# Optimization experiments

Measured on AMD Instinct MI355X. Metric: run time of the kernel, lower is better.

The kernel has to match this reference:

```python
import jax, jax.numpy as jnp
import numpy as np

N_NODES = 50000
N_EDGES = 800000
VOCAB = 4096          # node_emb_size
EMB_DIM = 128         # node_emb_dim
HIDDEN = 128          # hidden_dim -> layer1 out = 2*HIDDEN
N_POS = 1024


def gcn_conv(h, edge_index, W, b, n):
    """PyG GCNConv: lin -> add self loops -> sym-normalized scatter-add -> +bias."""
    h = h @ W                                   # [N, out]
    row, col = edge_index[0], edge_index[1]     # source, target
    loop = jnp.arange(n)
    row = jnp.concatenate([row, loop])
    col = jnp.concatenate([col, loop])
    deg = jax.ops.segment_sum(jnp.ones(row.shape[0], dtype=h.dtype), col, num_segments=n)
    dinv = jnp.where(deg > 0, jax.lax.rsqrt(deg), 0.0)
    norm = dinv[row] * dinv[col]                # [E+N]
    msg = h[row] * norm[:, None]                # gather + scale
    return jax.ops.segment_sum(msg, col, num_segments=n) + b


def setup_inputs() -> dict:
    key = jax.random.key(0)
    ks = jax.random.split(key, 10)
    x = jax.random.randint(ks[0], (N_NODES, 1), 0, VOCAB)
    edge_index = jax.random.randint(ks[1], (2, N_EDGES), 0, N_NODES)
    x_position = jax.random.randint(ks[2], (N_POS,), 0, N_NODES)
    # Embedding init: normal(0, emb_dim^-0.5) per initialize_parameters
    emb = jax.random.normal(ks[3], (VOCAB, EMB_DIM), jnp.float32) * EMB_DIM ** -0.5
    # GCN / linear weights (glorot-ish)
    W1 = jax.random.normal(ks[4], (EMB_DIM, 2 * HIDDEN), jnp.float32) * (EMB_DIM ** -0.5)
    b1 = jnp.zeros((2 * HIDDEN,), jnp.float32)
    W2 = jax.random.normal(ks[5], (2 * HIDDEN, HIDDEN), jnp.float32) * ((2 * HIDDEN) ** -0.5)
    b2 = jnp.zeros((HIDDEN,), jnp.float32)
    Wc = jax.random.normal(ks[6], (HIDDEN, VOCAB), jnp.float32) * (HIDDEN ** -0.5)
    bc = jnp.zeros((VOCAB,), jnp.float32)
    return {"x": x, "edge_index": edge_index, "x_position": x_position,
            "emb": emb, "W1": W1, "b1": b1, "W2": W2, "b2": b2, "Wc": Wc, "bc": bc}


def reference(x, edge_index, x_position, emb, W1, b1, W2, b2, Wc, bc):
    n = x.shape[0]
    h = emb[x[:, 0]]                                   # Embedding + squeeze(1)
    h = jax.nn.relu(gcn_conv(h, edge_index, W1, b1, n))
    z = gcn_conv(h, edge_index, W2, b2, n)             # [N, HIDDEN]
    logits = z @ Wc + bc                               # classifier over all nodes
    # embedding stage: mean of classified rows at x_position, keep dim 0
    return jnp.mean(logits[x_position], axis=0, keepdims=True)  # [1, VOCAB]
```

## Files before the change

### kernel.cpp

```cpp
#include <hip/hip_runtime.h>

constexpr int EMB  = 128;
constexpr int H1D  = 256;
constexpr int H2D  = 128;
constexpr int VOC  = 4096;
constexpr int NSL  = 32;

__global__ void k_init(int* cnt, int* count, unsigned int* needed, float* wagg,
                       float* wsum, int* nflag, int* total, int n, int nwords) {
    int i = blockIdx.x * blockDim.x + threadIdx.x;
    if (i < n) { cnt[i] = 0; count[i] = 0; wagg[i] = 0.0f; }
    if (i < nwords) needed[i] = 0u;
    if (i < NSL * H1D) wsum[i] = 0.0f;
    if (i == 0) { *nflag = 0; *total = 0; }
}

__global__ void k_count(const int* __restrict__ xpos, int* count, int np) {
    int p = blockIdx.x * blockDim.x + threadIdx.x;
    if (p < np) atomicAdd(&count[xpos[p]], 1);
}

__global__ void k_hist(const int* __restrict__ row, const int* __restrict__ col,
                       const int* __restrict__ count, int* cnt,
                       unsigned int* needed, int ne) {
    int e = blockIdx.x * blockDim.x + threadIdx.x;
    if (e < ne) {
        int c = col[e];
        atomicAdd(&cnt[c], 1);
        if (count[c] > 0) {
            int r = row[e];
            atomicOr(&needed[r >> 5], 1u << (r & 31));
        }
    }
}

__global__ void k_alloc(const unsigned int* __restrict__ needed,
                        const int* __restrict__ cnt, const int* __restrict__ count,
                        float* wagg, int* needb,
                        int* needlist, int* nflag, int* total,
                        int* offs, int* cursor, int n) {
    int v = blockIdx.x * blockDim.x + threadIdx.x;
    int lane = threadIdx.x & 63;
    int cv = 0;
    bool need = false;
    if (v < n) {
        cv = cnt[v];
        int cc = count[v];
        bool bit = (needed[v >> 5] >> (v & 31)) & 1u;
        bool flag = (cc > 0);
        need = bit || flag;
        needb[v] = need ? 1 : 0;
        if (flag) wagg[v] = (float)cc / ((float)cv + 1.0f);
    }
    int seg = need ? cv : 0;
    int incl = seg;
#pragma unroll
    for (int d = 1; d < 64; d <<= 1) {
        int t = __shfl_up(incl, d);
        if (lane >= d) incl += t;
    }
    int excl = incl - seg;
    int wave_total = __shfl(incl, 63);
    unsigned long long mask = __ballot(need);
    int rank = __popcll(mask & ((1ull << lane) - 1));
    int wcnt = __popcll(mask);
    int base_id = 0, base_off = 0;
    if (lane == 0) {
        if (wcnt > 0) base_id = atomicAdd(nflag, wcnt);
        if (wave_total > 0) base_off = atomicAdd(total, wave_total);
    }
    base_id  = __shfl(base_id, 0);
    base_off = __shfl(base_off, 0);
    if (need) {
        needlist[base_id + rank] = v;
        int o = base_off + excl;
        offs[v] = o;
        cursor[v] = o;
    }
}

__global__ void k_scatter(const int* __restrict__ row, const int* __restrict__ col,
                          const int* __restrict__ needb, const int* __restrict__ count,
                          const int* __restrict__ x, const int* __restrict__ cnt,
                          int* cursor, int* srowx, float* srowd, float* wagg, int ne) {
    int e = blockIdx.x * blockDim.x + threadIdx.x;
    if (e < ne) {
        int c = col[e];
        if (needb[c]) {
            int r = row[e];
            int pos = atomicAdd(&cursor[c], 1);
            float dr = rsqrtf((float)cnt[r] + 1.0f);
            srowx[pos] = x[r];
            srowd[pos] = dr;
            int cc = count[c];
            if (cc > 0) {
                float dc = rsqrtf((float)cnt[c] + 1.0f);
                atomicAdd(&wagg[r], (float)cc * dc * dr);
            }
        }
    }
}

constexpr int RPB = 16;
__global__ void k_embW1(const float* __restrict__ emb, const float* __restrict__ W1,
                        float* __restrict__ embW1) {
    __shared__ float er[RPB][EMB];
    int t = threadIdx.x;
    int r0 = blockIdx.x * RPB;
    for (int i = t; i < RPB * EMB; i += 256) {
        er[i / EMB][i % EMB] = emb[(size_t)r0 * EMB + i];
    }
    __syncthreads();
    float acc[RPB];
#pragma unroll
    for (int rr = 0; rr < RPB; rr++) acc[rr] = 0.0f;
    for (int k = 0; k < EMB; k++) {
        float w = W1[k * H1D + t];
#pragma unroll
        for (int rr = 0; rr < RPB; rr++) acc[rr] += er[rr][k] * w;
    }
#pragma unroll
    for (int rr = 0; rr < RPB; rr++) {
        embW1[(size_t)(r0 + rr) * H1D + t] = acc[rr];
    }
}

__global__ void k_fconv(const int* __restrict__ needlist, const int* __restrict__ nneed_p,
                        const float* __restrict__ wagg, const int* __restrict__ x,
                        const int* __restrict__ srowx, const float* __restrict__ srowd,
                        const int* __restrict__ offs, const int* __restrict__ cnt,
                        const float* __restrict__ embW1, const float* __restrict__ b1,
                        float* __restrict__ wsum) {
    int lane = threadIdx.x & 63;
    int wib  = threadIdx.x >> 6;
    int wid  = blockIdx.x * (blockDim.x >> 6) + wib;
    int nw   = gridDim.x * (blockDim.x >> 6);
    int nn   = *nneed_p;
    const float4* __restrict__ ew = (const float4*)embW1;
    float4 bfrag = ((const float4*)b1)[lane];
    float4 acc2 = {0.0f, 0.0f, 0.0f, 0.0f};

    for (int i = wid; i < nn; i += nw) {
        int v = needlist[i];
        int cv = cnt[v];
        float dv = rsqrtf((float)cv + 1.0f);
        float wa = wagg[v];
        float4 s = ew[(size_t)x[v] * 64 + lane];
        float w0 = dv * dv;
        float4 acc;
        acc.x = bfrag.x + w0 * s.x;
        acc.y = bfrag.y + w0 * s.y;
        acc.z = bfrag.z + w0 * s.z;
        acc.w = bfrag.w + w0 * s.w;
        int start = offs[v], m = cv;
        for (int base = 0; base < m; base += 64) {
            int mm = min(64, m - base);
            int xr = 0; float wr = 0.0f;
            if (lane < mm) {
                xr = srowx[start + base + lane];
                wr = srowd[start + base + lane] * dv;
            }
            int e = 0;
            for (; e + 4 <= mm; e += 4) {
                int i0 = __shfl(xr, e),     i1 = __shfl(xr, e + 1);
                int i2 = __shfl(xr, e + 2), i3 = __shfl(xr, e + 3);
                float q0 = __shfl(wr, e),     q1 = __shfl(wr, e + 1);
                float q2 = __shfl(wr, e + 2), q3 = __shfl(wr, e + 3);
                float4 t0 = ew[(size_t)i0 * 64 + lane];
                float4 t1 = ew[(size_t)i1 * 64 + lane];
                float4 t2 = ew[(size_t)i2 * 64 + lane];
                float4 t3 = ew[(size_t)i3 * 64 + lane];
                acc.x += q0 * t0.x + q1 * t1.x + q2 * t2.x + q3 * t3.x;
                acc.y += q0 * t0.y + q1 * t1.y + q2 * t2.y + q3 * t3.y;
                acc.z += q0 * t0.z + q1 * t1.z + q2 * t2.z + q3 * t3.z;
                acc.w += q0 * t0.w + q1 * t1.w + q2 * t2.w + q3 * t3.w;
            }
            for (; e < mm; e++) {
                int i0 = __shfl(xr, e);
                float q0 = __shfl(wr, e);
                float4 t0 = ew[(size_t)i0 * 64 + lane];
                acc.x += q0 * t0.x;
                acc.y += q0 * t0.y;
                acc.z += q0 * t0.z;
                acc.w += q0 * t0.w;
            }
        }
        acc2.x += wa * fmaxf(acc.x, 0.0f);
        acc2.y += wa * fmaxf(acc.y, 0.0f);
        acc2.z += wa * fmaxf(acc.z, 0.0f);
        acc2.w += wa * fmaxf(acc.w, 0.0f);
    }

    __shared__ float red[4][H1D];
    red[wib][4 * lane + 0] = acc2.x;
    red[wib][4 * lane + 1] = acc2.y;
    red[wib][4 * lane + 2] = acc2.z;
    red[wib][4 * lane + 3] = acc2.w;
    __syncthreads();
    int t = threadIdx.x;
    float ssum = red[0][t] + red[1][t] + red[2][t] + red[3][t];
    atomicAdd(&wsum[(blockIdx.x & (NSL - 1)) * H1D + t], ssum);
}

__global__ void k_zout(const float* __restrict__ wsum, const float* __restrict__ W2,
                       const float* __restrict__ b2, const float* __restrict__ Wc,
                       const float* __restrict__ bc, float* __restrict__ out,
                       float inv_np) {
    __shared__ float ws[H1D];
    __shared__ float z[H2D];
    int t = threadIdx.x;
    float s = 0.0f;
#pragma unroll
    for (int c = 0; c < NSL; c++) s += wsum[c * H1D + t];
    ws[t] = s;
    __syncthreads();
    if (t < H2D) {
        float acc = 0.0f;
#pragma unroll 8
        for (int k = 0; k < H1D; k++) acc += ws[k] * W2[k * H2D + t];
        z[t] = b2[t] + acc * inv_np;
    }
    __syncthreads();
    int c = blockIdx.x * blockDim.x + t;
    float acc = bc[c];
#pragma unroll 8
    for (int j = 0; j < H2D; j++) acc += z[j] * Wc[(size_t)j * VOC + c];
    out[c] = acc;
}

extern "C" void kernel_launch(void* const* d_in, const int* in_sizes, int n_in,
                              void* d_out, int out_size, void* d_ws, size_t ws_size,
                              hipStream_t stream) {
    const int n  = in_sizes[0];
    const int ne = in_sizes[1] / 2;
    const int np = in_sizes[2];

    const int*   x    = (const int*)d_in[0];
    const int*   ei   = (const int*)d_in[1];
    const int*   xpos = (const int*)d_in[2];
    const float* emb  = (const float*)d_in[3];
    const float* W1   = (const float*)d_in[4];
    const float* b1   = (const float*)d_in[5];
    const float* W2   = (const float*)d_in[6];
    const float* b2   = (const float*)d_in[7];
    const float* Wc   = (const float*)d_in[8];
    const float* bc   = (const float*)d_in[9];
    float*       out  = (float*)d_out;

    const int* row = ei;
    const int* col = ei + ne;

    char* p = (char*)d_ws;
    auto alloc = [&](size_t bytes) {
        char* r = p;
        p += (bytes + 255) & ~(size_t)255;
        return r;
    };
    int*          cnt      = (int*)alloc((size_t)n * 4);
    int*          offs     = (int*)alloc((size_t)n * 4);
    int*          cursor   = (int*)alloc((size_t)n * 4);
    int*          count    = (int*)alloc((size_t)n * 4);
    int*          needb    = (int*)alloc((size_t)n * 4);
    int*          needlist = (int*)alloc((size_t)n * 4);
    unsigned int* needed   = (unsigned int*)alloc((size_t)((n + 31) / 32) * 4);
    int*          srowx    = (int*)alloc((size_t)ne * 4);
    float*        srowd    = (float*)alloc((size_t)ne * 4);
    int*          nflag    = (int*)alloc(256 * 4);
    int*          total    = (int*)alloc(256 * 4);
    float*        wagg     = (float*)alloc((size_t)n * 4);
    float*        embW1    = (float*)alloc((size_t)VOC * H1D * 4);
    float*        wsum     = (float*)alloc((size_t)NSL * H1D * 4);

    const int nb     = (n + 255) / 256;
    const int neb    = (ne + 255) / 256;
    const int nwords = (n + 31) / 32;

    k_init<<<nb, 256, 0, stream>>>(cnt, count, needed, wagg, wsum, nflag, total, n, nwords);
    k_count<<<(np + 255) / 256, 256, 0, stream>>>(xpos, count, np);
    k_hist<<<neb, 256, 0, stream>>>(row, col, count, cnt, needed, ne);
    k_alloc<<<nb, 256, 0, stream>>>(needed, cnt, count, wagg, needb,
                                    needlist, nflag, total, offs, cursor, n);
    k_scatter<<<neb, 256, 0, stream>>>(row, col, needb, count, x, cnt,
                                       cursor, srowx, srowd, wagg, ne);
    k_embW1<<<VOC / RPB, 256, 0, stream>>>(emb, W1, embW1);
    k_fconv<<<2048, 256, 0, stream>>>(needlist, nflag, wagg, x, srowx, srowd, offs, cnt,
                                      embW1, b1, wsum);
    k_zout<<<VOC / 256, 256, 0, stream>>>(wsum, W2, b2, Wc, bc, out, 1.0f / (float)np);
}
```

Baseline: 194.6 us.

## Fuse count into embW1 kernel, use bitmasks for flags, pack edge records

Merges the x_position counting into the emb@W1 kernel as an extra block and removes one launch. Per-node 'need' and 'flag' int arrays become bitmasks, and k_alloc rewrites the mark bits in place as need bits via ballot. Source index and degree are packed into one int2 so k_fconv does a single 8-byte load per edge. Scatter and hist now read compact bitmasks instead of int arrays, which cuts memory traffic in the edge passes at the cost of some bit arithmetic.

```diff
diff --git a/kernel.cpp b/kernel.cpp
--- a/kernel.cpp
+++ b/kernel.cpp
@@ -6,38 +6,68 @@
 constexpr int VOC  = 4096;
 constexpr int NSL  = 32;
 
-__global__ void k_init(int* cnt, int* count, unsigned int* needed, float* wagg,
-                       float* wsum, int* nflag, int* total, int n, int nwords) {
+__global__ void k_init(int* cnt, int* count, unsigned int* flagbits, unsigned int* markw,
+                       float* wagg, float* wsum, int* nflag, int* total,
+                       int n, int nwords) {
     int i = blockIdx.x * blockDim.x + threadIdx.x;
     if (i < n) { cnt[i] = 0; count[i] = 0; wagg[i] = 0.0f; }
-    if (i < nwords) needed[i] = 0u;
+    if (i < nwords) { flagbits[i] = 0u; markw[i] = 0u; }
     if (i < NSL * H1D) wsum[i] = 0.0f;
     if (i == 0) { *nflag = 0; *total = 0; }
 }
 
-__global__ void k_count(const int* __restrict__ xpos, int* count, int np) {
-    int p = blockIdx.x * blockDim.x + threadIdx.x;
-    if (p < np) atomicAdd(&count[xpos[p]], 1);
+constexpr int RPB = 16;
+__global__ void k_embW1C(const float* __restrict__ emb, const float* __restrict__ W1,
+                         float* __restrict__ embW1,
+                         const int* __restrict__ xpos, int* count,
+                         unsigned int* flagbits, int np) {
+    int t = threadIdx.x;
+    if (blockIdx.x == VOC / RPB) {
+        for (int p = t; p < np; p += blockDim.x) {
+            int v = xpos[p];
+            atomicAdd(&count[v], 1);
+            atomicOr(&flagbits[v >> 5], 1u << (v & 31));
+        }
+        return;
+    }
+    __shared__ float er[RPB][EMB];
+    int r0 = blockIdx.x * RPB;
+    for (int i = t; i < RPB * EMB; i += 256) {
+        er[i / EMB][i % EMB] = emb[(size_t)r0 * EMB + i];
+    }
+    __syncthreads();
+    float acc[RPB];
+#pragma unroll
+    for (int rr = 0; rr < RPB; rr++) acc[rr] = 0.0f;
+    for (int k = 0; k < EMB; k++) {
+        float w = W1[k * H1D + t];
+#pragma unroll
+        for (int rr = 0; rr < RPB; rr++) acc[rr] += er[rr][k] * w;
+    }
+#pragma unroll
+    for (int rr = 0; rr < RPB; rr++) {
+        embW1[(size_t)(r0 + rr) * H1D + t] = acc[rr];
+    }
 }
 
 __global__ void k_hist(const int* __restrict__ row, const int* __restrict__ col,
-                       const int* __restrict__ count, int* cnt,
-                       unsigned int* needed, int ne) {
+                       const unsigned int* __restrict__ flagbits, int* cnt,
+                       unsigned int* markw, int ne) {
     int e = blockIdx.x * blockDim.x + threadIdx.x;
     if (e < ne) {
         int c = col[e];
         atomicAdd(&cnt[c], 1);
-        if (count[c] > 0) {
+        if ((flagbits[c >> 5] >> (c & 31)) & 1u) {
             int r = row[e];
-            atomicOr(&needed[r >> 5], 1u << (r & 31));
-        }
-    }
-}
-
-__global__ void k_alloc(const unsigned int* __restrict__ needed,
+            atomicOr(&markw[r >> 5], 1u << (r & 31));
+        }
+    }
+}
+
+__global__ void k_alloc(unsigned int* needw,
+                        const unsigned int* __restrict__ flagbits,
                         const int* __restrict__ cnt, const int* __restrict__ count,
-                        float* wagg, int* needb,
-                        int* needlist, int* nflag, int* total,
+                        float* wagg, int* needlist, int* nflag, int* total,
                         int* offs, int* cursor, int n) {
     int v = blockIdx.x * blockDim.x + threadIdx.x;
     int lane = threadIdx.x & 63;
@@ -45,13 +75,15 @@
     bool need = false;
     if (v < n) {
         cv = cnt[v];
-        int cc = count[v];
-        bool bit = (needed[v >> 5] >> (v & 31)) & 1u;
-        bool flag = (cc > 0);
-        need = bit || flag;
-        needb[v] = need ? 1 : 0;
-        if (flag) wagg[v] = (float)cc / ((float)cv + 1.0f);
-    }
+        bool mark = (needw[v >> 5] >> (v & 31)) & 1u;
+        bool flag = (flagbits[v >> 5] >> (v & 31)) & 1u;
+        need = mark || flag;
+        if (flag) wagg[v] = (float)count[v] / ((float)cv + 1.0f);
+    }
+    unsigned long long nm = __ballot(need);
+    int wbase = (v & ~63) >> 5;
+    if (lane == 0)  needw[wbase]     = (unsigned int)(nm & 0xffffffffu);
+    if (lane == 32) needw[wbase + 1] = (unsigned int)(nm >> 32);
     int seg = need ? cv : 0;
     int incl = seg;
 #pragma unroll
@@ -61,9 +93,8 @@
     }
     int excl = incl - seg;
     int wave_total = __shfl(incl, 63);
-    unsigned long long mask = __ballot(need);
-    int rank = __popcll(mask & ((1ull << lane) - 1));
-    int wcnt = __popcll(mask);
+    int rank = __popcll(nm & ((1ull << lane) - 1));
+    int wcnt = __popcll(nm);
     int base_id = 0, base_off = 0;
     if (lane == 0) {
         if (wcnt > 0) base_id = atomicAdd(nflag, wcnt);
@@ -80,54 +111,31 @@
 }
 
 __global__ void k_scatter(const int* __restrict__ row, const int* __restrict__ col,
-                          const int* __restrict__ needb, const int* __restrict__ count,
+                          const unsigned int* __restrict__ needw,
+                          const unsigned int* __restrict__ flagbits,
+                          const int* __restrict__ count,
                           const int* __restrict__ x, const int* __restrict__ cnt,
-                          int* cursor, int* srowx, float* srowd, float* wagg, int ne) {
+                          int* cursor, int2* srowp, float* wagg, int ne) {
     int e = blockIdx.x * blockDim.x + threadIdx.x;
     if (e < ne) {
         int c = col[e];
-        if (needb[c]) {
+        if ((needw[c >> 5] >> (c & 31)) & 1u) {
             int r = row[e];
             int pos = atomicAdd(&cursor[c], 1);
             float dr = rsqrtf((float)cnt[r] + 1.0f);
-            srowx[pos] = x[r];
-            srowd[pos] = dr;
-            int cc = count[c];
-            if (cc > 0) {
+            int2 pk; pk.x = x[r]; pk.y = __float_as_int(dr);
+            srowp[pos] = pk;
+            if ((flagbits[c >> 5] >> (c & 31)) & 1u) {
                 float dc = rsqrtf((float)cnt[c] + 1.0f);
-                atomicAdd(&wagg[r], (float)cc * dc * dr);
-            }
-        }
-    }
-}
-
-constexpr int RPB = 16;
-__global__ void k_embW1(const float* __restrict__ emb, const float* __restrict__ W1,
-                        float* __restrict__ embW1) {
-    __shared__ float er[RPB][EMB];
-    int t = threadIdx.x;
-    int r0 = blockIdx.x * RPB;
-    for (int i = t; i < RPB * EMB; i += 256) {
-        er[i / EMB][i % EMB] = emb[(size_t)r0 * EMB + i];
-    }
-    __syncthreads();
-    float acc[RPB];
-#pragma unroll
-    for (int rr = 0; rr < RPB; rr++) acc[rr] = 0.0f;
-    for (int k = 0; k < EMB; k++) {
-        float w = W1[k * H1D + t];
-#pragma unroll
-        for (int rr = 0; rr < RPB; rr++) acc[rr] += er[rr][k] * w;
-    }
-#pragma unroll
-    for (int rr = 0; rr < RPB; rr++) {
-        embW1[(size_t)(r0 + rr) * H1D + t] = acc[rr];
+                atomicAdd(&wagg[r], (float)count[c] * dc * dr);
+            }
+        }
     }
 }
 
 __global__ void k_fconv(const int* __restrict__ needlist, const int* __restrict__ nneed_p,
                         const float* __restrict__ wagg, const int* __restrict__ x,
-                        const int* __restrict__ srowx, const float* __restrict__ srowd,
+                        const int2* __restrict__ srowp,
                         const int* __restrict__ offs, const int* __restrict__ cnt,
                         const float* __restrict__ embW1, const float* __restrict__ b1,
                         float* __restrict__ wsum) {
@@ -157,8 +165,9 @@
             int mm = min(64, m - base);
             int xr = 0; float wr = 0.0f;
             if (lane < mm) {
-                xr = srowx[start + base + lane];
-                wr = srowd[start + base + lane] * dv;
+                int2 pk = srowp[start + base + lane];
+                xr = pk.x;
+                wr = __int_as_float(pk.y) * dv;
             }
             int e = 0;
             for (; e + 4 <= mm; e += 4) {
@@ -256,34 +265,33 @@
         p += (bytes + 255) & ~(size_t)255;
         return r;
     };
+    const int nb     = (n + 255) / 256;
+    const int neb    = (ne + 255) / 256;
+    const int nwords = nb * 8;
+
     int*          cnt      = (int*)alloc((size_t)n * 4);
     int*          offs     = (int*)alloc((size_t)n * 4);
     int*          cursor   = (int*)alloc((size_t)n * 4);
     int*          count    = (int*)alloc((size_t)n * 4);
-    int*          needb    = (int*)alloc((size_t)n * 4);
     int*          needlist = (int*)alloc((size_t)n * 4);
-    unsigned int* needed   = (unsigned int*)alloc((size_t)((n + 31) / 32) * 4);
-    int*          srowx    = (int*)alloc((size_t)ne * 4);
-    float*        srowd    = (float*)alloc((size_t)ne * 4);
+    unsigned int* needw    = (unsigned int*)alloc((size_t)nwords * 4);
+    unsigned int* flagbits = (unsigned int*)alloc((size_t)nwords * 4);
+    int2*         srowp    = (int2*)alloc((size_t)ne * 8);
     int*          nflag    = (int*)alloc(256 * 4);
     int*          total    = (int*)alloc(256 * 4);
     float*        wagg     = (float*)alloc((size_t)n * 4);
     float*        embW1    = (float*)alloc((size_t)VOC * H1D * 4);
     float*        wsum     = (float*)alloc((size_t)NSL * H1D * 4);
 
-    const int nb     = (n + 255) / 256;
-    const int neb    = (ne + 255) / 256;
-    const int nwords = (n + 31) / 32;
-
-    k_init<<<nb, 256, 0, stream>>>(cnt, count, needed, wagg, wsum, nflag, total, n, nwords);
-    k_count<<<(np + 255) / 256, 256, 0, stream>>>(xpos, count, np);
-    k_hist<<<neb, 256, 0, stream>>>(row, col, count, cnt, needed, ne);
-    k_alloc<<<nb, 256, 0, stream>>>(needed, cnt, count, wagg, needb,
+    k_init<<<nb, 256, 0, stream>>>(cnt, count, flagbits, needw, wagg, wsum,
+                                   nflag, total, n, nwords);
+    k_embW1C<<<VOC / RPB + 1, 256, 0, stream>>>(emb, W1, embW1, xpos, count, flagbits, np);
+    k_hist<<<neb, 256, 0, stream>>>(row, col, flagbits, cnt, needw, ne);
+    k_alloc<<<nb, 256, 0, stream>>>(needw, flagbits, cnt, count, wagg,
                                     needlist, nflag, total, offs, cursor, n);
-    k_scatter<<<neb, 256, 0, stream>>>(row, col, needb, count, x, cnt,
-                                       cursor, srowx, srowd, wagg, ne);
-    k_embW1<<<VOC / RPB, 256, 0, stream>>>(emb, W1, embW1);
-    k_fconv<<<2048, 256, 0, stream>>>(needlist, nflag, wagg, x, srowx, srowd, offs, cnt,
+    k_scatter<<<neb, 256, 0, stream>>>(row, col, needw, flagbits, count, x, cnt,
+                                       cursor, srowp, wagg, ne);
+    k_fconv<<<2048, 256, 0, stream>>>(needlist, nflag, wagg, x, srowp, offs, cnt,
                                       embW1, b1, wsum);
     k_zout<<<VOC / 256, 256, 0, stream>>>(wsum, W2, b2, Wc, bc, out, 1.0f / (float)np);
 }
```

After: 192.6 us. Within noise of the previous version (-1.0%).
